# Kernel optimization log

Measured on AMD Instinct MI355X. Metric: run time of the kernel, lower is better.

## Reference

```python
import jax, jax.numpy as jnp
import numpy as np

HIDDEN = 1024
QDIM = 16
B, S = 4, 2048
EPS = 1e-8


def setup_inputs() -> dict:
    key = jax.random.key(0)
    ks = jax.random.split(key, 12)
    sc_h = 1.0 / np.sqrt(HIDDEN)
    inp = {
        "x": jax.random.normal(ks[0], (B, S, HIDDEN), dtype=jnp.float32),
        "Wq": jax.random.normal(ks[1], (HIDDEN, HIDDEN), dtype=jnp.float32) * sc_h,
        "bq": jnp.zeros((HIDDEN,), dtype=jnp.float32),
        "Wk": jax.random.normal(ks[2], (HIDDEN, HIDDEN), dtype=jnp.float32) * sc_h,
        "bk": jnp.zeros((HIDDEN,), dtype=jnp.float32),
        "Wv": jax.random.normal(ks[3], (HIDDEN, HIDDEN), dtype=jnp.float32) * sc_h,
        "bv": jnp.zeros((HIDDEN,), dtype=jnp.float32),
        "We": jax.random.normal(ks[4], (HIDDEN, QDIM), dtype=jnp.float32) * sc_h,
        "be": jnp.zeros((QDIM,), dtype=jnp.float32),
        "Wo": jax.random.normal(ks[5], (HIDDEN, HIDDEN), dtype=jnp.float32) * sc_h,
        "bo": jnp.zeros((HIDDEN,), dtype=jnp.float32),
    }
    return inp


def _quantum_embed(h, We, be):
    # Linear projection to quantum amplitude space, then normalize to a unit state.
    z = h @ We + be                     # [..., QDIM]
    nrm = jnp.sqrt(jnp.sum(z * z, axis=-1, keepdims=True) + EPS)
    return z / nrm


def reference(x, Wq, bq, Wk, bk, Wv, bv, We, be, Wo, bo):
    # Projections
    q = x @ Wq + bq                     # [B,S,H]
    k = x @ Wk + bk
    v = x @ Wv + bv
    # Quantum state embeddings (unit-normalized amplitudes)
    q_q = _quantum_embed(q, We, be)     # [B,S,QDIM]
    k_q = _quantum_embed(k, We, be)
    # Quantum fidelity similarity |<q|k>|^2, vectorized over all pairs
    ov = jnp.einsum("bqd,bkd->bqk", q_q, k_q)   # [B,S,S]
    attn = jax.nn.softmax(ov * ov, axis=-1)
    attended = jnp.einsum("bqk,bkh->bqh", attn, v)
    return attended @ Wo + bo
```

## Files before the change

### kernel.cpp

```cpp
#include <hip/hip_runtime.h>

#define H 1024
#define QD 16
#define BATCH 4
#define SEQ 2048
#define MROWS 8192
#define KCH 64

typedef __bf16 bf16x8 __attribute__((ext_vector_type(8)));
typedef __bf16 bf16x4 __attribute__((ext_vector_type(4)));
typedef float f32x4 __attribute__((ext_vector_type(4)));

__device__ __forceinline__ void async_g2l_16(const void* g, void* l) {
  __builtin_amdgcn_global_load_lds(
      (const __attribute__((address_space(1))) unsigned int*)g,
      (__attribute__((address_space(3))) unsigned int*)l, 16, 0, 0);
}

__global__ __launch_bounds__(256) void cvt_split(const float* __restrict__ src,
                                                 __bf16* __restrict__ hi,
                                                 __bf16* __restrict__ lo, int n) {
  int i = (blockIdx.x * 256 + threadIdx.x) * 4;
  if (i < n) {
    float4 f = *(const float4*)(src + i);
    bf16x4 h, l;
    h[0] = (__bf16)f.x; l[0] = (__bf16)(f.x - (float)h[0]);
    h[1] = (__bf16)f.y; l[1] = (__bf16)(f.y - (float)h[1]);
    h[2] = (__bf16)f.z; l[2] = (__bf16)(f.z - (float)h[2]);
    h[3] = (__bf16)f.w; l[3] = (__bf16)(f.w - (float)h[3]);
    *(bf16x4*)(hi + i) = h;
    *(bf16x4*)(lo + i) = l;
  }
}

__global__ __launch_bounds__(256) void transpose_cvt_f32_bf16(
    const float* __restrict__ src, __bf16* __restrict__ dst, int R, int C) {
  __shared__ float t[32][33];
  const int rb = blockIdx.y * 32, cb = blockIdx.x * 32;
  const int c = threadIdx.x & 31;
  const int r0 = threadIdx.x >> 5;
#pragma unroll
  for (int rr = r0; rr < 32; rr += 8)
    t[rr][c] = src[(long)(rb + rr) * C + cb + c];
  __syncthreads();
#pragma unroll
  for (int rr = r0; rr < 32; rr += 8)
    dst[(long)(cb + rr) * R + rb + c] = (__bf16)t[c][rr];
}

__global__ __launch_bounds__(256) void k2_cqk(const float* __restrict__ Wq,
                                              const float* __restrict__ Wk,
                                              const float* __restrict__ We,
                                              __bf16* __restrict__ Cth,
                                              __bf16* __restrict__ Ctl) {
  const int gw = blockIdx.x * 4 + (threadIdx.x >> 6);
  const int lane = threadIdx.x & 63;
  const int mat = gw & 1, k = gw >> 1;
  const float* Wrow = (mat ? Wk : Wq) + (long)k * H;
  const int col = lane & 15, q4 = lane >> 4;
  const float* wp = Wrow + q4 * 256;
  const float* wep = We + (long)q4 * 256 * QD + col;
  float acc = 0.f;
#pragma unroll 4
  for (int n0 = 0; n0 < 256; n0 += 4) {
    float4 w4 = *(const float4*)(wp + n0);
    acc += w4.x * wep[(n0 + 0) * QD];
    acc += w4.y * wep[(n0 + 1) * QD];
    acc += w4.z * wep[(n0 + 2) * QD];
    acc += w4.w * wep[(n0 + 3) * QD];
  }
  acc += __shfl_xor(acc, 16);
  acc += __shfl_xor(acc, 32);
  if (lane < 16) {
    __bf16 hi = (__bf16)acc;
    __bf16 lo = (__bf16)(acc - (float)hi);
    long idx = (long)(mat * 16 + col) * H + k;
    Cth[idx] = hi;
    Ctl[idx] = lo;
  }
}

__global__ __launch_bounds__(512) void k2b_dvec(
    const float* __restrict__ bq, const float* __restrict__ bk,
    const float* __restrict__ We, const float* __restrict__ be,
    float* __restrict__ dvec) {
  __shared__ float part[16][32];
  const int tid = threadIdx.x;
  const int j = tid & 31, p = tid >> 5;
  const int mat = j >> 4, col = j & 15;
  const float* b = mat ? bk : bq;
  float acc = 0.f;
  for (int n = p * 64; n < p * 64 + 64; ++n) acc += b[n] * We[n * QD + col];
  part[p][j] = acc;
  __syncthreads();
  if (tid < 32) {
    float sum = be[tid & 15];
    for (int p2 = 0; p2 < 16; ++p2) sum += part[p2][tid];
    dvec[tid] = sum;
  }
}

__global__ __launch_bounds__(1024) void k3_embed_mfma(
    const __bf16* __restrict__ xh, const __bf16* __restrict__ xl,
    const __bf16* __restrict__ Cth, const __bf16* __restrict__ Ctl,
    const float* __restrict__ dvec, __bf16* __restrict__ qq32,
    __bf16* __restrict__ kk32) {
  __shared__ __bf16 Ah[4][32 * 64];
  __shared__ __bf16 Al[4][32 * 64];
  __shared__ __bf16 Bh[4][32 * 64];
  __shared__ __bf16 Bl[4][32 * 64];
  const int tid = threadIdx.x;
  const int lane = tid & 63;
  const int w = tid >> 6;
  const int kb = w >> 2;
  const int w4 = w & 3;
  const int rowhalf = w4 >> 1;
  const int ntile = w4 & 1;
  const int l15 = lane & 15, quad = lane >> 4;
  const long rowBase = (long)blockIdx.x * 32;

  const int half = tid >> 8;
  const int tl = tid & 255;
  const int srow = tl >> 3;
  const int seg = tl & 7;
  const int segsw = (seg ^ (srow & 7)) * 8;
  const long gk = half * 256 + segsw;
  const __bf16* agh = xh + (rowBase + srow) * H + gk;
  const __bf16* agl = xl + (rowBase + srow) * H + gk;
  const __bf16* bgh = Cth + (long)srow * H + gk;
  const __bf16* bgl = Ctl + (long)srow * H + gk;
  __bf16* lah = &Ah[half][srow * 64 + seg * 8];
  __bf16* lal = &Al[half][srow * 64 + seg * 8];
  __bf16* lbh = &Bh[half][srow * 64 + seg * 8];
  __bf16* lbl = &Bl[half][srow * 64 + seg * 8];

  f32x4 acc;
  acc[0] = 0.f; acc[1] = 0.f; acc[2] = 0.f; acc[3] = 0.f;
  const int arow = (rowhalf * 16 + l15) * 64;
  const int brow = (ntile * 16 + l15) * 64;
  const int h7 = l15 & 7;

  for (int k0 = 0; k0 < 256; k0 += 64) {
    async_g2l_16(agh + k0, lah);
    async_g2l_16(agl + k0, lal);
    async_g2l_16(bgh + k0, lbh);
    async_g2l_16(bgl + k0, lbl);
    __syncthreads();
#pragma unroll
    for (int s = 0; s < 2; ++s) {
      const int slot = ((s * 4 + quad) ^ h7) * 8;
      bf16x8 fah = *(const bf16x8*)&Ah[kb][arow + slot];
      bf16x8 fal = *(const bf16x8*)&Al[kb][arow + slot];
      bf16x8 fbh = *(const bf16x8*)&Bh[kb][brow + slot];
      bf16x8 fbl = *(const bf16x8*)&Bl[kb][brow + slot];
      acc = __builtin_amdgcn_mfma_f32_16x16x32_bf16(fah, fbh, acc, 0, 0, 0);
      acc = __builtin_amdgcn_mfma_f32_16x16x32_bf16(fal, fbh, acc, 0, 0, 0);
      acc = __builtin_amdgcn_mfma_f32_16x16x32_bf16(fah, fbl, acc, 0, 0, 0);
    }
    __syncthreads();
  }

  if (kb > 0) ((f32x4*)&Ah[kb][0])[w4 * 64 + lane] = acc;
  __syncthreads();
  if (kb == 0) {
#pragma unroll
    for (int q = 1; q < 4; ++q) {
      f32x4 o = ((const f32x4*)&Ah[q][0])[w4 * 64 + lane];
      acc[0] += o[0]; acc[1] += o[1]; acc[2] += o[2]; acc[3] += o[3];
    }
    const float dv = dvec[ntile * 16 + l15];
    const float osc = ntile ? 1.0f : 1.20112240878f;
    __bf16* outp = ntile ? kk32 : qq32;
#pragma unroll
    for (int r = 0; r < 4; ++r) {
      float z = acc[r] + dv;
      float s2 = z * z;
      s2 += __shfl_xor(s2, 1);
      s2 += __shfl_xor(s2, 2);
      s2 += __shfl_xor(s2, 4);
      s2 += __shfl_xor(s2, 8);
      float val = z * rsqrtf(s2 + 1e-8f) * osc;
      long row = rowBase + rowhalf * 16 + quad * 4 + r;
      outp[row * 32 + l15] = (__bf16)val;
      outp[row * 32 + 16 + l15] = (__bf16)0.f;
    }
  }
}

__global__ __launch_bounds__(512) void fused_attn(
    const __bf16* __restrict__ qq32, const __bf16* __restrict__ kk32,
    const __bf16* __restrict__ v_t, __bf16* __restrict__ attn) {
  __shared__ __bf16 Vlds[3][256 * KCH];
  __shared__ __bf16 Plds[2][128 * KCH];
  __shared__ float rsum2[128 * 2];
  const int tid = threadIdx.x;
  const int lane = tid & 63;
  const int w = tid >> 6;
  const int l15 = lane & 15, quad = lane >> 4;
  const int ws_k = w & 1, ws_q = w >> 1;
  const int wp_h = w & 3, wp_q = w >> 2;

  const int bid = blockIdx.x;
  const int xcd = bid & 7, s = bid >> 3;
  const int panel = xcd * 2 + (s >> 4);
  const int b = panel >> 2;
  const long hbase = (long)(panel & 3) * 256;
  const long qbase = (long)(s & 15) * 128;

  bf16x8 bq[2];
  {
    const __bf16* qqp =
        qq32 + ((long)b * SEQ + qbase + ws_q * 32 + l15) * 32 + quad * 8;
    bq[0] = *(const bf16x8*)qqp;
    bq[1] = *(const bf16x8*)(qqp + 16 * 32);
  }
  const __bf16* kkb = kk32 + ((long)b * SEQ + ws_k * 32 + l15) * 32 + quad * 8;

  const int vR = tid >> 3;
  const int vSL = (tid & 7) ^ (vR & 7);
  const __bf16* vgbase = v_t + (long)b * H * SEQ + (hbase + vR) * SEQ + vSL * 8;

  f32x4 acc[4][4];
#pragma unroll
  for (int i = 0; i < 4; ++i)
#pragma unroll
    for (int j = 0; j < 4; ++j) {
      acc[i][j][0] = 0.f; acc[i][j][1] = 0.f; acc[i][j][2] = 0.f; acc[i][j][3] = 0.f;
    }
  float rsPart[2] = {0.f, 0.f};

#pragma unroll
  for (int j = 0; j < 4; ++j)
    async_g2l_16(vgbase + (long)j * 64 * SEQ, &Vlds[0][j * 64 * KCH + tid * 8]);
  bf16x8 ak[2];
  ak[0] = *(const bf16x8*)kkb;
  ak[1] = *(const bf16x8*)(kkb + 16 * 32);

  int vcur = 0, vnxt = 1;
  for (int t = 0; t < SEQ / KCH; ++t) {
    const int kn = ((t + 1) & (SEQ / KCH - 1)) * KCH;
#pragma unroll
    for (int j = 0; j < 4; ++j)
      async_g2l_16(vgbase + (long)j * 64 * SEQ + kn,
                   &Vlds[vnxt][j * 64 * KCH + tid * 8]);

    __bf16* Pw = Plds[t & 1];
#pragma unroll
    for (int i = 0; i < 2; ++i) {
#pragma unroll
      for (int n = 0; n < 2; ++n) {
        f32x4 s2v;
        s2v[0] = 0.f; s2v[1] = 0.f; s2v[2] = 0.f; s2v[3] = 0.f;
        s2v = __builtin_amdgcn_mfma_f32_16x16x32_bf16(ak[i], bq[n], s2v, 0, 0, 0);
        bf16x4 pw;
        float part = 0.f;
#pragma unroll
        for (int r = 0; r < 4; ++r) {
          float wgt = exp2f(s2v[r] * s2v[r]);
          part += wgt;
          pw[r] = (__bf16)wgt;
        }
        rsPart[n] += part;
        const int q = ws_q * 32 + n * 16 + l15;
        const int g = ws_k * 4 + i * 2 + (quad >> 1);
        *(bf16x4*)&Pw[q * KCH + ((g ^ (q & 7)) << 3) + (quad & 1) * 4] = pw;
      }
    }
    ak[0] = *(const bf16x8*)(kkb + (long)kn * 32);
    ak[1] = *(const bf16x8*)(kkb + (long)(kn + 16) * 32);

    asm volatile("s_waitcnt lgkmcnt(0)" ::: "memory");
    asm volatile("s_waitcnt vmcnt(6)" ::: "memory");
    __builtin_amdgcn_sched_barrier(0);
    __builtin_amdgcn_s_barrier();

    const __bf16* Vr = Vlds[vcur];
#pragma unroll
    for (int ks = 0; ks < 2; ++ks) {
      bf16x8 ap[4], bv[4];
#pragma unroll
      for (int i = 0; i < 4; ++i) {
        const int q = wp_q * 64 + i * 16 + l15;
        ap[i] = *(const bf16x8*)&Pw[q * KCH + (((ks * 4 + quad) ^ (q & 7)) << 3)];
      }
#pragma unroll
      for (int j = 0; j < 4; ++j) {
        const int vr = wp_h * 64 + j * 16 + l15;
        bv[j] = *(const bf16x8*)&Vr[vr * KCH + (((ks * 4 + quad) ^ (vr & 7)) << 3)];
      }
#pragma unroll
      for (int i = 0; i < 4; ++i)
#pragma unroll
        for (int j = 0; j < 4; ++j)
          acc[i][j] =
              __builtin_amdgcn_mfma_f32_16x16x32_bf16(ap[i], bv[j], acc[i][j], 0, 0, 0);
    }
    const int third = 3 - vcur - vnxt;
    vcur = vnxt;
    vnxt = third;
  }

#pragma unroll
  for (int n = 0; n < 2; ++n) {
    float vs = rsPart[n];
    vs += __shfl_xor(vs, 16);
    vs += __shfl_xor(vs, 32);
    if (lane < 16) rsum2[(ws_q * 32 + n * 16 + l15) * 2 + ws_k] = vs;
  }
  __syncthreads();

  float rinv[4][4];
#pragma unroll
  for (int i = 0; i < 4; ++i)
#pragma unroll
    for (int r = 0; r < 4; ++r) {
      int row = wp_q * 64 + i * 16 + quad * 4 + r;
      rinv[i][r] = 1.0f / (rsum2[row * 2] + rsum2[row * 2 + 1]);
    }

  __bf16* ob = attn + ((long)b * SEQ + qbase) * H + hbase;
#pragma unroll
  for (int i = 0; i < 4; ++i)
#pragma unroll
    for (int j = 0; j < 4; ++j) {
      const int colL = wp_h * 64 + j * 16 + l15;
#pragma unroll
      for (int r = 0; r < 4; ++r) {
        const int rowL = wp_q * 64 + i * 16 + quad * 4 + r;
        ob[(long)rowL * H + colL] = (__bf16)(acc[i][j][r] * rinv[i][r]);
      }
    }
}

template <int OUTMODE, int HASBIAS>
__global__ __launch_bounds__(256) void gemm_bt(
    const __bf16* __restrict__ A, const __bf16* __restrict__ Bt,
    void* __restrict__ Cout, const float* __restrict__ bias, int M, int N, int K) {
  __shared__ __bf16 Alds[128 * 64];
  __shared__ __bf16 Blds[128 * 64];
  const int tid = threadIdx.x;
  const int lane = tid & 63;
  const int w = tid >> 6;
  const int wm = w >> 1, wn = w & 1;
  const int l15 = lane & 15, quad = lane >> 4;
  const long rowBase = (long)blockIdx.y * 128;
  const long colBase = (long)blockIdx.x * 128;

  const int srow = lane >> 3;
  const int segsw = ((lane & 7) ^ srow) * 8;

  const __bf16* ag[4];
  const __bf16* bg[4];
  __bf16* as_[4];
  __bf16* bs_[4];
#pragma unroll
  for (int j = 0; j < 4; ++j) {
    int r = j * 32 + w * 8;
    ag[j] = A + (rowBase + r + srow) * (long)K + segsw;
    bg[j] = Bt + (colBase + r + srow) * (long)K + segsw;
    as_[j] = &Alds[r * 64 + (lane & 7) * 8];
    bs_[j] = &Blds[r * 64 + (lane & 7) * 8];
  }

  f32x4 acc[4][4];
#pragma unroll
  for (int i = 0; i < 4; ++i)
#pragma unroll
    for (int j = 0; j < 4; ++j) {
      acc[i][j][0] = 0.f; acc[i][j][1] = 0.f; acc[i][j][2] = 0.f; acc[i][j][3] = 0.f;
    }

  const int h7 = l15 & 7;

  for (int k0 = 0; k0 < K; k0 += 64) {
#pragma unroll
    for (int j = 0; j < 4; ++j) {
      async_g2l_16(ag[j], as_[j]);
      async_g2l_16(bg[j], bs_[j]);
      ag[j] += 64;
      bg[j] += 64;
    }
    __syncthreads();
#pragma unroll
    for (int s = 0; s < 2; ++s) {
      const int slot = ((s * 4 + quad) ^ h7) * 8;
      bf16x8 af[4], bfv[4];
#pragma unroll
      for (int i = 0; i < 4; ++i) {
        af[i] = *(const bf16x8*)&Alds[(wm * 64 + i * 16 + l15) * 64 + slot];
        bfv[i] = *(const bf16x8*)&Blds[(wn * 64 + i * 16 + l15) * 64 + slot];
      }
#pragma unroll
      for (int i = 0; i < 4; ++i)
#pragma unroll
        for (int j = 0; j < 4; ++j)
          acc[i][j] =
              __builtin_amdgcn_mfma_f32_16x16x32_bf16(af[i], bfv[j], acc[i][j], 0, 0, 0);
    }
    __syncthreads();
  }

  const long crow0 = rowBase + wm * 64 + quad * 4;
  const long ccol0 = colBase + wn * 64 + l15;
#pragma unroll
  for (int i = 0; i < 4; ++i) {
#pragma unroll
    for (int j = 0; j < 4; ++j) {
      long col = ccol0 + j * 16;
      float bb = HASBIAS ? bias[col] : 0.f;
      if (OUTMODE == 2) {
        long row0 = crow0 + i * 16;
        int bz = (int)(row0 >> 11);
        long rb = row0 & (SEQ - 1);
        bf16x4 pv;
#pragma unroll
        for (int r = 0; r < 4; ++r) pv[r] = (__bf16)(acc[i][j][r] + bb);
        *(bf16x4*)&((__bf16*)Cout)[((long)bz * N + col) * SEQ + rb] = pv;
      } else {
#pragma unroll
        for (int r = 0; r < 4; ++r) {
          long row = crow0 + i * 16 + r;
          float val = acc[i][j][r] + bb;
          if (OUTMODE == 0)
            ((float*)Cout)[row * N + col] = val;
          else
            ((__bf16*)Cout)[row * N + col] = (__bf16)val;
        }
      }
    }
  }
}

extern "C" void kernel_launch(void* const* d_in, const int* in_sizes, int n_in,
                              void* d_out, int out_size, void* d_ws, size_t ws_size,
                              hipStream_t stream) {
  const float* x = (const float*)d_in[0];
  const float* Wq = (const float*)d_in[1];
  const float* bq = (const float*)d_in[2];
  const float* Wk = (const float*)d_in[3];
  const float* bk = (const float*)d_in[4];
  const float* Wv = (const float*)d_in[5];
  const float* bv = (const float*)d_in[6];
  const float* We = (const float*)d_in[7];
  const float* be = (const float*)d_in[8];
  const float* Wo = (const float*)d_in[9];
  const float* bo = (const float*)d_in[10];
  float* out = (float*)d_out;

  char* ws = (char*)d_ws;
  size_t o = 0;
  auto alloc = [&](size_t n) {
    size_t r = o;
    o += (n + 255) & ~(size_t)255;
    return r;
  };
  __bf16* xbf = (__bf16*)(ws + alloc((size_t)MROWS * H * 2));
  __bf16* v_t = (__bf16*)(ws + alloc((size_t)MROWS * H * 2));
  __bf16* attn = (__bf16*)(ws + alloc((size_t)MROWS * H * 2));
  __bf16* Wvt = (__bf16*)(ws + alloc((size_t)H * H * 2));
  __bf16* Wot = (__bf16*)(ws + alloc((size_t)H * H * 2));
  __bf16* Cth = (__bf16*)(ws + alloc((size_t)32 * H * 2));
  __bf16* Ctl = (__bf16*)(ws + alloc((size_t)32 * H * 2));
  float* dvec = (float*)(ws + alloc(32 * 4));
  __bf16* qq32 = (__bf16*)(ws + alloc((size_t)MROWS * 32 * 2));
  __bf16* kk32 = (__bf16*)(ws + alloc((size_t)MROWS * 32 * 2));
  __bf16* xlo = attn;
  if (ws_size < o) return;

  cvt_split<<<MROWS * H / 1024, 256, 0, stream>>>(x, xbf, xlo, MROWS * H);
  transpose_cvt_f32_bf16<<<dim3(32, 32), 256, 0, stream>>>(Wv, Wvt, H, H);
  transpose_cvt_f32_bf16<<<dim3(32, 32), 256, 0, stream>>>(Wo, Wot, H, H);
  k2_cqk<<<512, 256, 0, stream>>>(Wq, Wk, We, Cth, Ctl);
  k2b_dvec<<<1, 512, 0, stream>>>(bq, bk, We, be, dvec);
  k3_embed_mfma<<<MROWS / 32, 1024, 0, stream>>>(xbf, xlo, Cth, Ctl, dvec, qq32, kk32);
  gemm_bt<2, 1><<<dim3(8, 64), 256, 0, stream>>>(xbf, Wvt, v_t, bv, MROWS, H, H);
  fused_attn<<<256, 512, 0, stream>>>(qq32, kk32, v_t, attn);
  gemm_bt<0, 1><<<dim3(8, 64), 256, 0, stream>>>(attn, Wot, out, bo, MROWS, H, H);
}
```

Before: 240.5 us.

## Double fused attention block to 1024 threads and swizzle GEMM blocks per XCD

The fused attention kernel now runs 16 waves per block instead of 8. Each wave handles half as many query rows for the score computation and the P·V accumulation, and each thread issues two async V loads instead of four, which halves the accumulator registers per thread and adds latency hiding. Separately, the GEMM kernel remaps its flat block id so that blocks landing on the same XCD share row panels, aiming for better L2 reuse of A. The larger block raises barrier cost and may hurt scheduling, but it lowers register pressure.

```diff
diff --git a/kernel.cpp b/kernel.cpp
--- a/kernel.cpp
+++ b/kernel.cpp
@@ -187,7 +187,7 @@
   }
 }
 
-__global__ __launch_bounds__(512) void fused_attn(
+__global__ __launch_bounds__(1024) void fused_attn(
     const __bf16* __restrict__ qq32, const __bf16* __restrict__ kk32,
     const __bf16* __restrict__ v_t, __bf16* __restrict__ attn) {
   __shared__ __bf16 Vlds[3][256 * KCH];
@@ -197,7 +197,7 @@
   const int lane = tid & 63;
   const int w = tid >> 6;
   const int l15 = lane & 15, quad = lane >> 4;
-  const int ws_k = w & 1, ws_q = w >> 1;
+  const int sq = w >> 1, sk = w & 1;
   const int wp_h = w & 3, wp_q = w >> 2;
 
   const int bid = blockIdx.x;
@@ -207,31 +207,26 @@
   const long hbase = (long)(panel & 3) * 256;
   const long qbase = (long)(s & 15) * 128;
 
-  bf16x8 bq[2];
-  {
-    const __bf16* qqp =
-        qq32 + ((long)b * SEQ + qbase + ws_q * 32 + l15) * 32 + quad * 8;
-    bq[0] = *(const bf16x8*)qqp;
-    bq[1] = *(const bf16x8*)(qqp + 16 * 32);
-  }
-  const __bf16* kkb = kk32 + ((long)b * SEQ + ws_k * 32 + l15) * 32 + quad * 8;
+  const bf16x8 bq = *(const bf16x8*)(qq32 +
+      ((long)b * SEQ + qbase + sq * 16 + l15) * 32 + quad * 8);
+  const __bf16* kkb = kk32 + ((long)b * SEQ + sk * 32 + l15) * 32 + quad * 8;
 
   const int vR = tid >> 3;
   const int vSL = (tid & 7) ^ (vR & 7);
-  const __bf16* vgbase = v_t + (long)b * H * SEQ + (hbase + vR) * SEQ + vSL * 8;
-
-  f32x4 acc[4][4];
-#pragma unroll
-  for (int i = 0; i < 4; ++i)
+  const __bf16* vg0 = v_t + (long)b * H * SEQ + (hbase + vR) * SEQ + vSL * 8;
+  const __bf16* vg1 = vg0 + (long)128 * SEQ;
+
+  f32x4 acc[2][4];
+#pragma unroll
+  for (int i = 0; i < 2; ++i)
 #pragma unroll
     for (int j = 0; j < 4; ++j) {
       acc[i][j][0] = 0.f; acc[i][j][1] = 0.f; acc[i][j][2] = 0.f; acc[i][j][3] = 0.f;
     }
-  float rsPart[2] = {0.f, 0.f};
-
-#pragma unroll
-  for (int j = 0; j < 4; ++j)
-    async_g2l_16(vgbase + (long)j * 64 * SEQ, &Vlds[0][j * 64 * KCH + tid * 8]);
+  float rsPart = 0.f;
+
+  async_g2l_16(vg0, &Vlds[0][vR * KCH + (tid & 7) * 8]);
+  async_g2l_16(vg1, &Vlds[0][(vR + 128) * KCH + (tid & 7) * 8]);
   bf16x8 ak[2];
   ak[0] = *(const bf16x8*)kkb;
   ak[1] = *(const bf16x8*)(kkb + 16 * 32);
@@ -239,48 +234,43 @@
   int vcur = 0, vnxt = 1;
   for (int t = 0; t < SEQ / KCH; ++t) {
     const int kn = ((t + 1) & (SEQ / KCH - 1)) * KCH;
-#pragma unroll
-    for (int j = 0; j < 4; ++j)
-      async_g2l_16(vgbase + (long)j * 64 * SEQ + kn,
-                   &Vlds[vnxt][j * 64 * KCH + tid * 8]);
+    async_g2l_16(vg0 + kn, &Vlds[vnxt][vR * KCH + (tid & 7) * 8]);
+    async_g2l_16(vg1 + kn, &Vlds[vnxt][(vR + 128) * KCH + (tid & 7) * 8]);
 
     __bf16* Pw = Plds[t & 1];
 #pragma unroll
     for (int i = 0; i < 2; ++i) {
-#pragma unroll
-      for (int n = 0; n < 2; ++n) {
-        f32x4 s2v;
-        s2v[0] = 0.f; s2v[1] = 0.f; s2v[2] = 0.f; s2v[3] = 0.f;
-        s2v = __builtin_amdgcn_mfma_f32_16x16x32_bf16(ak[i], bq[n], s2v, 0, 0, 0);
-        bf16x4 pw;
-        float part = 0.f;
-#pragma unroll
-        for (int r = 0; r < 4; ++r) {
-          float wgt = exp2f(s2v[r] * s2v[r]);
-          part += wgt;
-          pw[r] = (__bf16)wgt;
-        }
-        rsPart[n] += part;
-        const int q = ws_q * 32 + n * 16 + l15;
-        const int g = ws_k * 4 + i * 2 + (quad >> 1);
-        *(bf16x4*)&Pw[q * KCH + ((g ^ (q & 7)) << 3) + (quad & 1) * 4] = pw;
-      }
+      f32x4 s2v;
+      s2v[0] = 0.f; s2v[1] = 0.f; s2v[2] = 0.f; s2v[3] = 0.f;
+      s2v = __builtin_amdgcn_mfma_f32_16x16x32_bf16(ak[i], bq, s2v, 0, 0, 0);
+      bf16x4 pw;
+      float part = 0.f;
+#pragma unroll
+      for (int r = 0; r < 4; ++r) {
+        float wgt = exp2f(s2v[r] * s2v[r]);
+        part += wgt;
+        pw[r] = (__bf16)wgt;
+      }
+      rsPart += part;
+      const int q = sq * 16 + l15;
+      const int g = sk * 4 + i * 2 + (quad >> 1);
+      *(bf16x4*)&Pw[q * KCH + ((g ^ (q & 7)) << 3) + (quad & 1) * 4] = pw;
     }
     ak[0] = *(const bf16x8*)(kkb + (long)kn * 32);
     ak[1] = *(const bf16x8*)(kkb + (long)(kn + 16) * 32);
 
     asm volatile("s_waitcnt lgkmcnt(0)" ::: "memory");
-    asm volatile("s_waitcnt vmcnt(6)" ::: "memory");
+    asm volatile("s_waitcnt vmcnt(4)" ::: "memory");
     __builtin_amdgcn_sched_barrier(0);
     __builtin_amdgcn_s_barrier();
 
     const __bf16* Vr = Vlds[vcur];
 #pragma unroll
     for (int ks = 0; ks < 2; ++ks) {
-      bf16x8 ap[4], bv[4];
-#pragma unroll
-      for (int i = 0; i < 4; ++i) {
-        const int q = wp_q * 64 + i * 16 + l15;
+      bf16x8 ap[2], bv[4];
+#pragma unroll
+      for (int i = 0; i < 2; ++i) {
+        const int q = wp_q * 32 + i * 16 + l15;
         ap[i] = *(const bf16x8*)&Pw[q * KCH + (((ks * 4 + quad) ^ (q & 7)) << 3)];
       }
 #pragma unroll
@@ -289,7 +279,7 @@
         bv[j] = *(const bf16x8*)&Vr[vr * KCH + (((ks * 4 + quad) ^ (vr & 7)) << 3)];
       }
 #pragma unroll
-      for (int i = 0; i < 4; ++i)
+      for (int i = 0; i < 2; ++i)
 #pragma unroll
         for (int j = 0; j < 4; ++j)
           acc[i][j] =
@@ -300,33 +290,32 @@
     vnxt = third;
   }
 
-#pragma unroll
-  for (int n = 0; n < 2; ++n) {
-    float vs = rsPart[n];
+  {
+    float vs = rsPart;
     vs += __shfl_xor(vs, 16);
     vs += __shfl_xor(vs, 32);
-    if (lane < 16) rsum2[(ws_q * 32 + n * 16 + l15) * 2 + ws_k] = vs;
+    if (lane < 16) rsum2[(sq * 16 + l15) * 2 + sk] = vs;
   }
   __syncthreads();
 
-  float rinv[4][4];
-#pragma unroll
-  for (int i = 0; i < 4; ++i)
+  float rinv[2][4];
+#pragma unroll
+  for (int i = 0; i < 2; ++i)
 #pragma unroll
     for (int r = 0; r < 4; ++r) {
-      int row = wp_q * 64 + i * 16 + quad * 4 + r;
+      int row = wp_q * 32 + i * 16 + quad * 4 + r;
       rinv[i][r] = 1.0f / (rsum2[row * 2] + rsum2[row * 2 + 1]);
     }
 
   __bf16* ob = attn + ((long)b * SEQ + qbase) * H + hbase;
 #pragma unroll
-  for (int i = 0; i < 4; ++i)
+  for (int i = 0; i < 2; ++i)
 #pragma unroll
     for (int j = 0; j < 4; ++j) {
       const int colL = wp_h * 64 + j * 16 + l15;
 #pragma unroll
       for (int r = 0; r < 4; ++r) {
-        const int rowL = wp_q * 64 + i * 16 + quad * 4 + r;
+        const int rowL = wp_q * 32 + i * 16 + quad * 4 + r;
         ob[(long)rowL * H + colL] = (__bf16)(acc[i][j][r] * rinv[i][r]);
       }
     }
@@ -343,8 +332,13 @@
   const int w = tid >> 6;
   const int wm = w >> 1, wn = w & 1;
   const int l15 = lane & 15, quad = lane >> 4;
-  const long rowBase = (long)blockIdx.y * 128;
-  const long colBase = (long)blockIdx.x * 128;
+
+  const int flat = blockIdx.y * 8 + blockIdx.x;
+  const int xcd = flat & 7, idx = flat >> 3;
+  const int rowPanel = xcd * 8 + (idx >> 3);
+  const int colBlk = idx & 7;
+  const long rowBase = (long)rowPanel * 128;
+  const long colBase = (long)colBlk * 128;
 
   const int srow = lane >> 3;
   const int segsw = ((lane & 7) ^ srow) * 8;
@@ -474,6 +468,6 @@
   k2b_dvec<<<1, 512, 0, stream>>>(bq, bk, We, be, dvec);
   k3_embed_mfma<<<MROWS / 32, 1024, 0, stream>>>(xbf, xlo, Cth, Ctl, dvec, qq32, kk32);
   gemm_bt<2, 1><<<dim3(8, 64), 256, 0, stream>>>(xbf, Wvt, v_t, bv, MROWS, H, H);
-  fused_attn<<<256, 512, 0, stream>>>(qq32, kk32, v_t, attn);
+  fused_attn<<<256, 1024, 0, stream>>>(qq32, kk32, v_t, attn);
   gemm_bt<0, 1><<<dim3(8, 64), 256, 0, stream>>>(attn, Wot, out, bo, MROWS, H, H);
 }
```

Measured after the change: 235.1 us. 2.2% less time.
